# Performance work log

Measured on AMD Instinct MI355X. Metric: run time of the kernel, lower is better.

The kernel has to match this reference:

```python
import math
import jax, jax.numpy as jnp
import numpy as np

H = 1024      # d_model
NHALF = 32    # N // 2
L_LEN = 4096
DT_MIN, DT_MAX = 1e-3, 1e-1


def setup_inputs() -> dict:
    key = jax.random.key(0)
    k1, k2 = jax.random.split(key)
    # C stored as real view of a complex (H, N/2) tensor -> (H, N/2, 2)
    C_ri = jax.random.normal(k1, (H, NHALF, 2), dtype=jnp.float32)
    # log_dt ~ Uniform(log(dt_min), log(dt_max))
    u = jax.random.uniform(k2, (H,), dtype=jnp.float32)
    log_dt = u * (math.log(DT_MAX) - math.log(DT_MIN)) + math.log(DT_MIN)
    # log_A_real = log(0.5 * ones), A_imag = pi * arange(N/2) broadcast over H
    log_A_real = jnp.full((H, NHALF), math.log(0.5), dtype=jnp.float32)
    A_imag = math.pi * jnp.broadcast_to(jnp.arange(NHALF, dtype=jnp.float32), (H, NHALF))
    A_imag = jnp.asarray(A_imag)
    return {"C_ri": C_ri, "log_dt": log_dt, "log_A_real": log_A_real,
            "A_imag": A_imag, "L": L_LEN}


def reference(C_ri, log_dt, log_A_real, A_imag, L):
    dt = jnp.exp(log_dt)                              # (H,)
    C = C_ri[..., 0] + 1j * C_ri[..., 1]              # (H, n) complex
    A = -jnp.exp(log_A_real) + 1j * A_imag            # (H, n) complex
    dtA = A * dt[:, None]                             # (H, n)
    # Vandermonde: exp(dtA * l) for l in [0, L)  -> (H, n, L) complex
    coeffs = dtA[:, :, None] * jnp.arange(L, dtype=jnp.float32)
    lhs = C * (jnp.exp(dtA) - 1.0) / A                # (H, n)
    K_complex = jnp.einsum('hn,hnl->hl', lhs, jnp.exp(coeffs))
    return 2.0 * K_complex.real                       # (H, L) float32
```

## Files before the change

kernel.cpp:

```cpp
#include <hip/hip_runtime.h>
#include <math.h>

#define HDIM 1024
#define NH 32
#define LLEN 4096
#define NT 256
#define QN 64
#define RN 64
#define LDK 72

typedef __attribute__((ext_vector_type(8))) short bf16x8;
typedef __attribute__((ext_vector_type(4))) float f32x4;

__device__ __forceinline__ unsigned short f2bf(float x) {
    unsigned int u = __builtin_bit_cast(unsigned int, x);
    unsigned int r = (u + 0x7FFFu + ((u >> 16) & 1u)) >> 16;
    return (unsigned short)r;
}
__device__ __forceinline__ float bf2f(unsigned short h) {
    unsigned int u = ((unsigned int)h) << 16;
    return __builtin_bit_cast(float, u);
}

__global__ __launch_bounds__(NT, 4) void s4d_kernel(
    const float* __restrict__ C_ri,
    const float* __restrict__ log_dt,
    const float* __restrict__ log_A_real,
    const float* __restrict__ A_imag,
    float* __restrict__ out)
{
    __shared__ float s_hi[NH], s_lo[NH], s_re2[NH], s_lr[NH], s_li[NH];
    __shared__ unsigned short sAh[QN][LDK], sAl[QN][LDK];
    __shared__ unsigned short sBh[RN][LDK], sBl[RN][LDK];

    const int h = blockIdx.x;
    const int tid = threadIdx.x;

    if (tid < NH) {
        const int n = tid;
        const int hn = h * NH + n;

        const float dt = expf(log_dt[h]);
        const float Ar = -expf(log_A_real[hn]);
        const float Ai = A_imag[hn];
        const float dtAr = Ar * dt;
        const float dtAi = Ai * dt;

        const float er = expf(dtAr);
        float sn, cs;
        sincosf(dtAi, &sn, &cs);
        const float Er = er * cs - 1.0f;
        const float Ei = er * sn;
        const float cr = C_ri[2 * hn + 0];
        const float ci = C_ri[2 * hn + 1];
        const float nr = cr * Er - ci * Ei;
        const float ni = cr * Ei + ci * Er;
        const float inv = 1.0f / (Ar * Ar + Ai * Ai);
        s_lr[n] = (nr * Ar + ni * Ai) * inv;
        s_li[n] = (ni * Ar - nr * Ai) * inv;

        const float re2 = dtAr * 1.4426950408889634f;
        s_re2[n] = re2;
        const double sd = (double)dtAi * 0.15915494309189535;
        const double fd = sd - floor(sd);
        const float hi = (float)(floor(fd * 4096.0 + 0.5) * (1.0 / 4096.0));
        s_hi[n] = hi;
        s_lo[n] = (float)(fd - (double)hi);
    }
    __syncthreads();

#pragma unroll
    for (int k = 0; k < 16; ++k) {
        const int e = tid + NT * k;
        const int isB = e >> 11;
        const int idx = e & 2047;
        const int n = idx & 31;
        const int row = idx >> 5;
        const float m = (float)(isB ? row : row * 64);

        const float x = s_hi[n] * m;
        const float fr = x - floorf(x);
        float rev = fmaf(s_lo[n], m, fr);
        rev -= floorf(rev);
        const float ev = exp2f(s_re2[n] * m);
        const float zr = ev * __builtin_amdgcn_cosf(rev);
        const float zi = ev * __builtin_amdgcn_sinf(rev);

        float ar, ai;
        if (isB) {
            ar = zr; ai = zi;
        } else {
            const float lr = s_lr[n], li = s_li[n];
            ar =  2.0f * (lr * zr - li * zi);
            ai = -2.0f * (lr * zi + li * zr);
        }

        const unsigned short hr = f2bf(ar);
        const unsigned short hj = f2bf(ai);
        const unsigned short lr2 = f2bf(ar - bf2f(hr));
        const unsigned short lj2 = f2bf(ai - bf2f(hj));
        const unsigned int hpack = (unsigned int)hr | ((unsigned int)hj << 16);
        const unsigned int lpack = (unsigned int)lr2 | ((unsigned int)lj2 << 16);
        if (isB) {
            *(unsigned int*)&sBh[row][2 * n] = hpack;
            *(unsigned int*)&sBl[row][2 * n] = lpack;
        } else {
            *(unsigned int*)&sAh[row][2 * n] = hpack;
            *(unsigned int*)&sAl[row][2 * n] = lpack;
        }
    }
    __syncthreads();

    const int wv = tid >> 6;
    const int lane = tid & 63;
    const int li16 = lane & 15;
    const int lg = lane >> 4;

    f32x4 acc[4];
#pragma unroll
    for (int tc = 0; tc < 4; ++tc) acc[tc] = (f32x4){0.f, 0.f, 0.f, 0.f};

#pragma unroll
    for (int s = 0; s < 6; ++s) {
        const unsigned short (*Am)[LDK] = (s >= 4) ? sAl : sAh;
        const unsigned short (*Bm)[LDK] = (s == 2 || s == 3) ? sBl : sBh;
        const int kb = (s & 1) * 32;
        const int ko = kb + 8 * lg;

        const bf16x8 af = *(const bf16x8*)&Am[16 * wv + li16][ko];
#pragma unroll
        for (int tc = 0; tc < 4; ++tc) {
            const bf16x8 bfr = *(const bf16x8*)&Bm[16 * tc + li16][ko];
            acc[tc] = __builtin_amdgcn_mfma_f32_16x16x32_bf16(af, bfr, acc[tc], 0, 0, 0);
        }
    }

    const int obase = h * LLEN;
#pragma unroll
    for (int tc = 0; tc < 4; ++tc) {
        const int r = 16 * tc + li16;
#pragma unroll
        for (int reg = 0; reg < 4; ++reg) {
            const int q = 16 * wv + 4 * lg + reg;
            out[obase + 64 * q + r] = acc[tc][reg];
        }
    }
}

extern "C" void kernel_launch(void* const* d_in, const int* in_sizes, int n_in,
                              void* d_out, int out_size, void* d_ws, size_t ws_size,
                              hipStream_t stream) {
    const float* C_ri       = (const float*)d_in[0];
    const float* log_dt     = (const float*)d_in[1];
    const float* log_A_real = (const float*)d_in[2];
    const float* A_imag     = (const float*)d_in[3];
    float* out = (float*)d_out;

    s4d_kernel<<<dim3(HDIM), dim3(NT), 0, stream>>>(C_ri, log_dt, log_A_real, A_imag, out);
}
```

Measured before the change: 14.33 us.

## Swap GEMM operand roles for vectorized float4 stores and drop shared-param sync

Every thread now computes its own per-mode parameters instead of 32 threads writing them to shared memory, which removes a __syncthreads and the shared-memory reads. The fine-step factors (row offsets) become the A operand and the coarse, lhs-scaled factors become B. This transposes the accumulator layout so each lane writes four contiguous outputs with one float4 store instead of scalar strided stores. The bf16 hi/lo split now truncates instead of rounding to nearest, which is cheaper but gives a slightly larger split error. The cost is redundant transcendental and double-precision math in all 256 threads.

```diff
diff --git a/kernel.cpp b/kernel.cpp
--- a/kernel.cpp
+++ b/kernel.cpp
@@ -5,20 +5,15 @@
 #define NH 32
 #define LLEN 4096
 #define NT 256
-#define QN 64
-#define RN 64
 #define LDK 72
 
 typedef __attribute__((ext_vector_type(8))) short bf16x8;
 typedef __attribute__((ext_vector_type(4))) float f32x4;
 
-__device__ __forceinline__ unsigned short f2bf(float x) {
-    unsigned int u = __builtin_bit_cast(unsigned int, x);
-    unsigned int r = (u + 0x7FFFu + ((u >> 16) & 1u)) >> 16;
-    return (unsigned short)r;
+__device__ __forceinline__ unsigned int fbits(float x) {
+    return __builtin_bit_cast(unsigned int, x);
 }
-__device__ __forceinline__ float bf2f(unsigned short h) {
-    unsigned int u = ((unsigned int)h) << 16;
+__device__ __forceinline__ float bitsf(unsigned int u) {
     return __builtin_bit_cast(float, u);
 }
 
@@ -29,85 +24,83 @@
     const float* __restrict__ A_imag,
     float* __restrict__ out)
 {
-    __shared__ float s_hi[NH], s_lo[NH], s_re2[NH], s_lr[NH], s_li[NH];
-    __shared__ unsigned short sAh[QN][LDK], sAl[QN][LDK];
-    __shared__ unsigned short sBh[RN][LDK], sBl[RN][LDK];
+    __shared__ unsigned short sAh[64][LDK], sAl[64][LDK];
+    __shared__ unsigned short sBh[64][LDK], sBl[64][LDK];
 
     const int h = blockIdx.x;
     const int tid = threadIdx.x;
+    const int n = tid & 31;
+    const int hn = h * NH + n;
+    const int r0 = tid >> 5;
 
-    if (tid < NH) {
-        const int n = tid;
-        const int hn = h * NH + n;
+    const float dt = expf(log_dt[h]);
+    const float Ar = -expf(log_A_real[hn]);
+    const float Ai = A_imag[hn];
+    const float dtAr = Ar * dt;
+    const float dtAi = Ai * dt;
 
-        const float dt = expf(log_dt[h]);
-        const float Ar = -expf(log_A_real[hn]);
-        const float Ai = A_imag[hn];
-        const float dtAr = Ar * dt;
-        const float dtAi = Ai * dt;
+    const float er = expf(dtAr);
+    float sn, cs;
+    sincosf(dtAi, &sn, &cs);
+    const float Er = er * cs - 1.0f;
+    const float Ei = er * sn;
+    const float cr = C_ri[2 * hn + 0];
+    const float ci = C_ri[2 * hn + 1];
+    const float nr = cr * Er - ci * Ei;
+    const float ni = cr * Ei + ci * Er;
+    const float inv = 1.0f / (Ar * Ar + Ai * Ai);
+    const float lr = (nr * Ar + ni * Ai) * inv;
+    const float li = (ni * Ar - nr * Ai) * inv;
 
-        const float er = expf(dtAr);
-        float sn, cs;
-        sincosf(dtAi, &sn, &cs);
-        const float Er = er * cs - 1.0f;
-        const float Ei = er * sn;
-        const float cr = C_ri[2 * hn + 0];
-        const float ci = C_ri[2 * hn + 1];
-        const float nr = cr * Er - ci * Ei;
-        const float ni = cr * Ei + ci * Er;
-        const float inv = 1.0f / (Ar * Ar + Ai * Ai);
-        s_lr[n] = (nr * Ar + ni * Ai) * inv;
-        s_li[n] = (ni * Ar - nr * Ai) * inv;
-
-        const float re2 = dtAr * 1.4426950408889634f;
-        s_re2[n] = re2;
-        const double sd = (double)dtAi * 0.15915494309189535;
-        const double fd = sd - floor(sd);
-        const float hi = (float)(floor(fd * 4096.0 + 0.5) * (1.0 / 4096.0));
-        s_hi[n] = hi;
-        s_lo[n] = (float)(fd - (double)hi);
-    }
-    __syncthreads();
+    const float re2 = dtAr * 1.4426950408889634f;
+    const double sd = (double)dtAi * 0.15915494309189535;
+    const double fdd = sd - floor(sd);
+    const float phi = (float)(floor(fdd * 4096.0 + 0.5) * (1.0 / 4096.0));
+    const float plo = (float)(fdd - (double)phi);
 
 #pragma unroll
-    for (int k = 0; k < 16; ++k) {
-        const int e = tid + NT * k;
-        const int isB = e >> 11;
-        const int idx = e & 2047;
-        const int n = idx & 31;
-        const int row = idx >> 5;
-        const float m = (float)(isB ? row : row * 64);
-
-        const float x = s_hi[n] * m;
+    for (int k = 0; k < 8; ++k) {
+        const int row = r0 + 8 * k;
+        const float m = (float)row;
+        const float x = phi * m;
         const float fr = x - floorf(x);
-        float rev = fmaf(s_lo[n], m, fr);
+        float rev = fmaf(plo, m, fr);
         rev -= floorf(rev);
-        const float ev = exp2f(s_re2[n] * m);
+        const float ev = exp2f(re2 * m);
         const float zr = ev * __builtin_amdgcn_cosf(rev);
         const float zi = ev * __builtin_amdgcn_sinf(rev);
 
-        float ar, ai;
-        if (isB) {
-            ar = zr; ai = zi;
-        } else {
-            const float lr = s_lr[n], li = s_li[n];
-            ar =  2.0f * (lr * zr - li * zi);
-            ai = -2.0f * (lr * zi + li * zr);
-        }
+        const unsigned int ur = fbits(zr), ui = fbits(zi);
+        const unsigned int hp = (ur >> 16) | (ui & 0xFFFF0000u);
+        const float rl = zr - bitsf(ur & 0xFFFF0000u);
+        const float il = zi - bitsf(ui & 0xFFFF0000u);
+        const unsigned int lp = (fbits(rl) >> 16) | (fbits(il) & 0xFFFF0000u);
+        *(unsigned int*)&sAh[row][2 * n] = hp;
+        *(unsigned int*)&sAl[row][2 * n] = lp;
+    }
 
-        const unsigned short hr = f2bf(ar);
-        const unsigned short hj = f2bf(ai);
-        const unsigned short lr2 = f2bf(ar - bf2f(hr));
-        const unsigned short lj2 = f2bf(ai - bf2f(hj));
-        const unsigned int hpack = (unsigned int)hr | ((unsigned int)hj << 16);
-        const unsigned int lpack = (unsigned int)lr2 | ((unsigned int)lj2 << 16);
-        if (isB) {
-            *(unsigned int*)&sBh[row][2 * n] = hpack;
-            *(unsigned int*)&sBl[row][2 * n] = lpack;
-        } else {
-            *(unsigned int*)&sAh[row][2 * n] = hpack;
-            *(unsigned int*)&sAl[row][2 * n] = lpack;
-        }
+#pragma unroll
+    for (int k = 0; k < 8; ++k) {
+        const int row = r0 + 8 * k;
+        const float m = (float)(row * 64);
+        const float x = phi * m;
+        const float fr = x - floorf(x);
+        float rev = fmaf(plo, m, fr);
+        rev -= floorf(rev);
+        const float ev = exp2f(re2 * m);
+        const float zr = ev * __builtin_amdgcn_cosf(rev);
+        const float zi = ev * __builtin_amdgcn_sinf(rev);
+
+        const float br = 2.0f * (lr * zr - li * zi);
+        const float bi = -2.0f * (lr * zi + li * zr);
+
+        const unsigned int ur = fbits(br), ui = fbits(bi);
+        const unsigned int hp = (ur >> 16) | (ui & 0xFFFF0000u);
+        const float rl = br - bitsf(ur & 0xFFFF0000u);
+        const float il = bi - bitsf(ui & 0xFFFF0000u);
+        const unsigned int lp = (fbits(rl) >> 16) | (fbits(il) & 0xFFFF0000u);
+        *(unsigned int*)&sBh[row][2 * n] = hp;
+        *(unsigned int*)&sBl[row][2 * n] = lp;
     }
     __syncthreads();
 
@@ -124,8 +117,7 @@
     for (int s = 0; s < 6; ++s) {
         const unsigned short (*Am)[LDK] = (s >= 4) ? sAl : sAh;
         const unsigned short (*Bm)[LDK] = (s == 2 || s == 3) ? sBl : sBh;
-        const int kb = (s & 1) * 32;
-        const int ko = kb + 8 * lg;
+        const int ko = (s & 1) * 32 + 8 * lg;
 
         const bf16x8 af = *(const bf16x8*)&Am[16 * wv + li16][ko];
 #pragma unroll
@@ -135,15 +127,11 @@
         }
     }
 
-    const int obase = h * LLEN;
+    const int base = h * LLEN + 64 * li16 + 16 * wv + 4 * lg;
 #pragma unroll
     for (int tc = 0; tc < 4; ++tc) {
-        const int r = 16 * tc + li16;
-#pragma unroll
-        for (int reg = 0; reg < 4; ++reg) {
-            const int q = 16 * wv + 4 * lg + reg;
-            out[obase + 64 * q + r] = acc[tc][reg];
-        }
+        *(float4*)&out[base + 1024 * tc] =
+            make_float4(acc[tc][0], acc[tc][1], acc[tc][2], acc[tc][3]);
     }
 }
 
```

Result: faster. 13.28 us (-7.3%).
